# Optimization experiments

Measured on AMD Instinct MI355X. Metric: run time of the kernel, lower is better.

Reference implementation:

```python
import jax, jax.numpy as jnp
import numpy as np

B = 16
COUNTS = np.array([6, 14, 10, 8, 16, 12, 9, 11, 7, 13, 10, 10, 8, 12, 6, 8], dtype=np.int64)  # sum=160, max=16
INPUT_DIM = 1024
D_IN = 834   # num_features_mixed4f + 2
G = 256      # num_features_gcn
NG = 4       # num_graphs
T, H, W = 8, 14, 14


def setup_inputs() -> dict:
    key = jax.random.key(0)
    ks = jax.random.split(key, 7)
    total = int(COUNTS.sum())
    return {
        "actor_features": jax.random.normal(ks[0], (total, INPUT_DIM), dtype=jnp.float32),
        "feature_map": jax.random.normal(ks[1], (B, D_IN, T, H, W), dtype=jnp.float32),
        "W_a": jax.random.normal(ks[2], (NG, G, INPUT_DIM), dtype=jnp.float32) * 0.02,
        "b_a": jnp.zeros((NG, G), dtype=jnp.float32),
        "W_c": jax.random.normal(ks[3], (NG, G, D_IN), dtype=jnp.float32) * 0.02,
        "b_c": jnp.zeros((NG, G), dtype=jnp.float32),
        "W_h": jax.random.normal(ks[4], (NG, G, G), dtype=jnp.float32) * 0.02,
        "num_actors_list": COUNTS,
        "return_features": 0,
    }


def _ragged_indices(counts):
    # static (concrete) ragged bookkeeping
    counts = np.asarray(counts)
    Bn = counts.shape[0]
    Nmax = int(counts.max())
    offsets = np.concatenate([np.zeros(1, np.int64), np.cumsum(counts)[:-1]])
    n = np.arange(Nmax)
    pad_idx = offsets[:, None] + np.minimum(n[None, :], counts[:, None] - 1)  # [B, Nmax]
    valid = (n[None, :] < counts[:, None])                                     # [B, Nmax]
    unpad_b = np.repeat(np.arange(Bn), counts)
    unpad_n = np.concatenate([np.arange(c) for c in counts])
    return pad_idx, valid, unpad_b, unpad_n


def reference(actor_features, feature_map, W_a, b_a, W_c, b_c, W_h,
              num_actors_list, return_features):
    pad_idx, valid, unpad_b, unpad_n = _ragged_indices(num_actors_list)
    valid_f = jnp.asarray(valid, actor_features.dtype)
    Bn = feature_map.shape[0]

    # actor embedding for all graphs: [total, ng, G]
    emb = jnp.einsum('td,gfd->tgf', actor_features, W_a) + b_a[None]
    # pad to [B, Nmax, ng, G]; zero padded slots (matches pad_sequence)
    padded = emb[pad_idx] * valid_f[:, :, None, None]

    # 1x1x1 conv == channel matmul over flattened spatio-temporal grid S=T*H*W
    fm = feature_map.reshape(Bn, feature_map.shape[1], -1)            # [B, C, S]
    ctx = jnp.einsum('bcs,gfc->bgfs', fm, W_c) + b_c[None, :, :, None]  # [B, ng, G, S]

    # adjacency: actor x context similarities, softmax over context locations
    adj = jnp.einsum('bngf,bgfs->bgns', padded, ctx)                  # [B, ng, Nmax, S]
    adj = jax.nn.softmax(adj, axis=-1)
    adj = adj * valid_f[:, None, :, None]                             # masked_fill pad rows -> 0

    # aggregate context + residual
    upd = jnp.einsum('bgns,bgfs->bngf', adj, ctx) + padded            # [B, Nmax, ng, G]

    # unpad back to ragged flat [total, ng, G] (dropout is identity in eval)
    flat = upd[unpad_b, unpad_n]
    out = jax.nn.relu(jnp.einsum('tgf,ghf->tgh', flat, W_h))          # head_linear + relu

    # func == 'concat': cat over graphs along feature dim -> [total, ng*G]
    return out.reshape(out.shape[0], -1)
```

## Files before the change

### kernel.cpp

```cpp
#include <hip/hip_runtime.h>

#define TOTAL   160
#define NMAX    16
#define INDIM   1024
#define DIN     834
#define KPAD    864
#define GF      256
#define SS      1568
#define SPAD    1664
#define CROW    264

__constant__ int c_counts[16] = {6,14,10,8,16,12,9,11,7,13,10,10,8,12,6,8};
__constant__ int c_offs[16]   = {0,6,20,30,38,54,66,75,86,93,106,116,126,134,146,152};
__constant__ int c_t0[4] = {0, 12, 24, 36};
__constant__ int c_t1[4] = {12, 24, 36, 49};

using bf16x8 = __attribute__((ext_vector_type(8))) short;
using f32x4  = __attribute__((ext_vector_type(4))) float;
using us4    = __attribute__((ext_vector_type(4))) unsigned short;

__device__ inline unsigned short f2bf(float f) {
  union { float f; unsigned u; } v; v.f = f;
  const unsigned u = v.u;
  return (unsigned short)((u + 0x7FFFu + ((u >> 16) & 1u)) >> 16);
}
__device__ inline float bf2f(unsigned short h) {
  union { unsigned u; float f; } v; v.u = ((unsigned)h) << 16; return v.f;
}

__global__ __launch_bounds__(256) void prep(const float* __restrict__ Wc,
                                            unsigned short* __restrict__ Ah,
                                            const float* __restrict__ Wh,
                                            unsigned short* __restrict__ Wh_h) {
  const int bid = blockIdx.x, tid = threadIdx.x;
  if (bid < 3456) {
    const int idx = bid * 256 + tid;
    const int k = idx % KPAD, gm = idx / KPAD;
    Ah[idx] = (k < DIN) ? f2bf(Wc[gm * DIN + k]) : (unsigned short)0;
  } else {
    const int i = (bid - 3456) * 256 + tid;
    const float4 v = reinterpret_cast<const float4*>(Wh)[i];
    us4 o; o[0] = f2bf(v.x); o[1] = f2bf(v.y); o[2] = f2bf(v.z); o[3] = f2bf(v.w);
    reinterpret_cast<us4*>(Wh_h)[i] = o;
  }
}

__global__ __launch_bounds__(256) void fm_to_bf16T(const float* __restrict__ fm,
                                                   unsigned short* __restrict__ BhT) {
  __shared__ float tile[32][33];
  const int b  = blockIdx.z;
  const int k0 = blockIdx.y * 32;
  const int s0 = blockIdx.x * 32;
  const int tx = threadIdx.x & 31, ty = threadIdx.x >> 5;
  const float* src = fm + (size_t)b * DIN * SS;
  #pragma unroll
  for (int r = 0; r < 4; ++r) {
    const int k = k0 + ty + r * 8;
    tile[ty + r * 8][tx] = (k < DIN) ? src[(size_t)k * SS + s0 + tx] : 0.f;
  }
  __syncthreads();
  unsigned short* dst = BhT + (size_t)b * SS * KPAD;
  #pragma unroll
  for (int r = 0; r < 4; ++r) {
    const int s = s0 + ty + r * 8;
    dst[(size_t)s * KPAD + k0 + tx] = f2bf(tile[tx][ty + r * 8]);
  }
}

__global__ __launch_bounds__(256, 3) void ctx_mfma(const unsigned short* __restrict__ Ah,
                                                   const unsigned short* __restrict__ BhT,
                                                   const float* __restrict__ b_c,
                                                   unsigned short* __restrict__ ctxT) {
  __shared__ unsigned short As[128 * 40];
  __shared__ unsigned short Bs[128 * 40];
  const int z = blockIdx.z, g = z >> 4, b = z & 15;
  const int n0 = blockIdx.x * 128;
  const int m0 = blockIdx.y * 128;
  const int tid = threadIdx.x;
  const int wave = tid >> 6, lane = tid & 63;
  const int wm = (wave >> 1) * 64, wn = (wave & 1) * 64;
  const int quad = lane >> 4, lr = lane & 15;

  const unsigned short* Ag = BhT + (size_t)b * SS * KPAD;
  const unsigned short* Bg = Ah + (size_t)g * 256 * KPAD + (size_t)n0 * KPAD;

  const int c0 = tid, c1 = tid + 256;
  const int r0 = c0 >> 2, ko0 = (c0 & 3) * 8;
  const int r1 = c1 >> 2, ko1 = (c1 & 3) * 8;

  f32x4 acc[4][4];
  #pragma unroll
  for (int i = 0; i < 4; ++i)
    #pragma unroll
    for (int j = 0; j < 4; ++j) acc[i][j] = (f32x4){0.f, 0.f, 0.f, 0.f};

  uint4 ra0, ra1, rb0, rb1;
  {
    ra0 = *reinterpret_cast<const uint4*>(Ag + (size_t)(m0 + r0) * KPAD + ko0);
    ra1 = *reinterpret_cast<const uint4*>(Ag + (size_t)(m0 + r1) * KPAD + ko1);
    rb0 = *reinterpret_cast<const uint4*>(Bg + (size_t)r0 * KPAD + ko0);
    rb1 = *reinterpret_cast<const uint4*>(Bg + (size_t)r1 * KPAD + ko1);
  }

  for (int kt = 0; kt < 27; ++kt) {
    __syncthreads();
    *reinterpret_cast<uint4*>(&As[r0 * 40 + ko0]) = ra0;
    *reinterpret_cast<uint4*>(&As[r1 * 40 + ko1]) = ra1;
    *reinterpret_cast<uint4*>(&Bs[r0 * 40 + ko0]) = rb0;
    *reinterpret_cast<uint4*>(&Bs[r1 * 40 + ko1]) = rb1;
    __syncthreads();
    if (kt < 26) {
      const int k0 = (kt + 1) * 32;
      ra0 = *reinterpret_cast<const uint4*>(Ag + (size_t)(m0 + r0) * KPAD + k0 + ko0);
      ra1 = *reinterpret_cast<const uint4*>(Ag + (size_t)(m0 + r1) * KPAD + k0 + ko1);
      rb0 = *reinterpret_cast<const uint4*>(Bg + (size_t)r0 * KPAD + k0 + ko0);
      rb1 = *reinterpret_cast<const uint4*>(Bg + (size_t)r1 * KPAD + k0 + ko1);
    }
    bf16x8 af[4], bfr[4];
    #pragma unroll
    for (int i = 0; i < 4; ++i)
      af[i] = *reinterpret_cast<const bf16x8*>(&As[(wm + i * 16 + lr) * 40 + quad * 8]);
    #pragma unroll
    for (int j = 0; j < 4; ++j)
      bfr[j] = *reinterpret_cast<const bf16x8*>(&Bs[(wn + j * 16 + lr) * 40 + quad * 8]);
    #pragma unroll
    for (int i = 0; i < 4; ++i)
      #pragma unroll
      for (int j = 0; j < 4; ++j)
        acc[i][j] = __builtin_amdgcn_mfma_f32_16x16x32_bf16(af[i], bfr[j], acc[i][j], 0, 0, 0);
  }

  unsigned short* Cz = ctxT + (size_t)z * SPAD * GF;
  const float* bias = b_c + g * GF;
  #pragma unroll
  for (int j = 0; j < 4; ++j) {
    const int n = n0 + wn + j * 16 + lr;
    const float bv = bias[n];
    #pragma unroll
    for (int i = 0; i < 4; ++i) {
      #pragma unroll
      for (int reg = 0; reg < 4; ++reg) {
        const int m = m0 + wm + i * 16 + quad * 4 + reg;
        Cz[(size_t)m * GF + n] = f2bf(acc[i][j][reg] + bv);
      }
    }
  }
}

__global__ __launch_bounds__(256) void emb_mfma(const float* __restrict__ actor,
                                                const float* __restrict__ Wa,
                                                const float* __restrict__ b_a,
                                                float* __restrict__ emb,
                                                unsigned short* __restrict__ emb_h) {
  __shared__ unsigned short As[64 * 40];
  __shared__ unsigned short Bs[64 * 40];
  const int n0 = blockIdx.x * 64, m0 = blockIdx.y * 64;
  const int tid = threadIdx.x;
  const int wave = tid >> 6, lane = tid & 63;
  const int wm = (wave >> 1) * 32, wn = (wave & 1) * 32;
  const int quad = lane >> 4, lr = lane & 15;
  const int r = tid >> 2, ko = (tid & 3) * 8;
  const bool mval = (m0 + r < TOTAL);

  f32x4 acc[2][2];
  #pragma unroll
  for (int i = 0; i < 2; ++i)
    #pragma unroll
    for (int j = 0; j < 2; ++j) acc[i][j] = (f32x4){0.f, 0.f, 0.f, 0.f};

  const float4 zf4 = {0.f, 0.f, 0.f, 0.f};
  float4 ra0, ra1, rb0, rb1;
  ra0 = mval ? *reinterpret_cast<const float4*>(actor + (size_t)(m0 + r) * INDIM + ko) : zf4;
  ra1 = mval ? *reinterpret_cast<const float4*>(actor + (size_t)(m0 + r) * INDIM + ko + 4) : zf4;
  rb0 = *reinterpret_cast<const float4*>(Wa + (size_t)(n0 + r) * INDIM + ko);
  rb1 = *reinterpret_cast<const float4*>(Wa + (size_t)(n0 + r) * INDIM + ko + 4);

  for (int kt = 0; kt < 32; ++kt) {
    __syncthreads();
    {
      us4 a0, a1, b0, b1;
      a0[0]=f2bf(ra0.x); a0[1]=f2bf(ra0.y); a0[2]=f2bf(ra0.z); a0[3]=f2bf(ra0.w);
      a1[0]=f2bf(ra1.x); a1[1]=f2bf(ra1.y); a1[2]=f2bf(ra1.z); a1[3]=f2bf(ra1.w);
      b0[0]=f2bf(rb0.x); b0[1]=f2bf(rb0.y); b0[2]=f2bf(rb0.z); b0[3]=f2bf(rb0.w);
      b1[0]=f2bf(rb1.x); b1[1]=f2bf(rb1.y); b1[2]=f2bf(rb1.z); b1[3]=f2bf(rb1.w);
      *reinterpret_cast<us4*>(&As[r * 40 + ko])     = a0;
      *reinterpret_cast<us4*>(&As[r * 40 + ko + 4]) = a1;
      *reinterpret_cast<us4*>(&Bs[r * 40 + ko])     = b0;
      *reinterpret_cast<us4*>(&Bs[r * 40 + ko + 4]) = b1;
    }
    __syncthreads();
    if (kt < 31) {
      const int k0 = (kt + 1) * 32;
      ra0 = mval ? *reinterpret_cast<const float4*>(actor + (size_t)(m0 + r) * INDIM + k0 + ko) : zf4;
      ra1 = mval ? *reinterpret_cast<const float4*>(actor + (size_t)(m0 + r) * INDIM + k0 + ko + 4) : zf4;
      rb0 = *reinterpret_cast<const float4*>(Wa + (size_t)(n0 + r) * INDIM + k0 + ko);
      rb1 = *reinterpret_cast<const float4*>(Wa + (size_t)(n0 + r) * INDIM + k0 + ko + 4);
    }
    bf16x8 af[2], bfr[2];
    #pragma unroll
    for (int i = 0; i < 2; ++i)
      af[i] = *reinterpret_cast<const bf16x8*>(&As[(wm + i * 16 + lr) * 40 + quad * 8]);
    #pragma unroll
    for (int j = 0; j < 2; ++j)
      bfr[j] = *reinterpret_cast<const bf16x8*>(&Bs[(wn + j * 16 + lr) * 40 + quad * 8]);
    #pragma unroll
    for (int i = 0; i < 2; ++i)
      #pragma unroll
      for (int j = 0; j < 2; ++j)
        acc[i][j] = __builtin_amdgcn_mfma_f32_16x16x32_bf16(af[i], bfr[j], acc[i][j], 0, 0, 0);
  }

  #pragma unroll
  for (int i = 0; i < 2; ++i) {
    #pragma unroll
    for (int reg = 0; reg < 4; ++reg) {
      const int m = m0 + wm + i * 16 + quad * 4 + reg;
      if (m >= TOTAL) continue;
      #pragma unroll
      for (int j = 0; j < 2; ++j) {
        const int n = n0 + wn + j * 16 + lr;
        const float v = acc[i][j][reg] + b_a[n];
        emb[(size_t)m * INDIM + n] = v;
        emb_h[(size_t)m * INDIM + n] = f2bf(v);
      }
    }
  }
}

__global__ __launch_bounds__(256) void att_part(
    const unsigned short* __restrict__ ctxT,
    const unsigned short* __restrict__ emb_h,
    float* __restrict__ Opart,
    float* __restrict__ Spart)
{
  __shared__ unsigned short Cs[4][32 * CROW];
  __shared__ float Ps[4][32][20];
  __shared__ float walpha[4][16];
  __shared__ float wms[4][16], wls[4][16];
  const int sc = blockIdx.x, z = blockIdx.y;
  const int g = z >> 4, b = z & 15;
  const int count = c_counts[b], off = c_offs[b];
  const int t0 = c_t0[sc], t1 = c_t1[sc];
  const int tid = threadIdx.x, wave = tid >> 6, lane = tid & 63;
  const int quad = lane >> 4, lr = lane & 15;
  const unsigned short* Az = ctxT + (size_t)z * SPAD * GF;
  const bool bvalid = (lr < count);
  const unsigned short* Brow = emb_h + (size_t)(off + (bvalid ? lr : 0)) * INDIM + (g << 8);
  unsigned short* myC = &Cs[wave][0];
  const int fbase = quad * 64 + lr * 4;
  const bf16x8 zero8 = (bf16x8)(short)0;

  float O[16][4];
  #pragma unroll
  for (int n = 0; n < 16; ++n)
    #pragma unroll
    for (int j = 0; j < 4; ++j) O[n][j] = 0.f;
  float m_run = -3.0e38f, l_run = 0.f;

  for (int t = t0 + wave; t < t1; t += 4) {
    const int s0 = t * 32;
    #pragma unroll
    for (int q = 0; q < 16; ++q) {
      const int row = 2 * q + (lane >> 5);
      const int col = (lane & 31) * 8;
      const uint4 v = *reinterpret_cast<const uint4*>(Az + (size_t)(s0 + row) * GF + col);
      *reinterpret_cast<uint4*>(&myC[row * CROW + col]) = v;
    }
    f32x4 acc[2] = {(f32x4){0.f,0.f,0.f,0.f}, (f32x4){0.f,0.f,0.f,0.f}};
    #pragma unroll
    for (int kk = 0; kk < 8; ++kk) {
      const int f = kk * 32 + quad * 8;
      bf16x8 bv8 = *reinterpret_cast<const bf16x8*>(Brow + f);
      if (!bvalid) bv8 = zero8;
      #pragma unroll
      for (int i = 0; i < 2; ++i) {
        const bf16x8 av8 = *reinterpret_cast<const bf16x8*>(&myC[(i * 16 + lr) * CROW + f]);
        acc[i] = __builtin_amdgcn_mfma_f32_16x16x32_bf16(av8, bv8, acc[i], 0, 0, 0);
      }
    }
    float mx = acc[0][0];
    #pragma unroll
    for (int i = 0; i < 2; ++i)
      #pragma unroll
      for (int r = 0; r < 4; ++r) mx = fmaxf(mx, acc[i][r]);
    float lsum = 0.f;
    #pragma unroll
    for (int i = 0; i < 2; ++i)
      #pragma unroll
      for (int r = 0; r < 4; ++r) lsum += __expf(acc[i][r] - mx);
    #pragma unroll
    for (int d = 16; d < 64; d <<= 1) {
      const float om = __shfl_xor(mx, d, 64);
      const float ol = __shfl_xor(lsum, d, 64);
      const float M = fmaxf(mx, om);
      lsum = lsum * __expf(mx - M) + ol * __expf(om - M);
      mx = M;
    }
    const float m_new = fmaxf(m_run, mx);
    const float alpha = __expf(m_run - m_new);
    const float beta  = __expf(mx - m_new);
    l_run = alpha * l_run + beta * lsum;
    m_run = m_new;
    if (lane < 16) walpha[wave][lane] = alpha;
    #pragma unroll
    for (int i = 0; i < 2; ++i)
      #pragma unroll
      for (int r = 0; r < 4; ++r) {
        const int sl = i * 16 + quad * 4 + r;
        Ps[wave][sl][lr] = beta * __expf(acc[i][r] - mx);
      }
    float av[16];
    {
      const float4 a0 = *reinterpret_cast<const float4*>(&walpha[wave][0]);
      const float4 a1 = *reinterpret_cast<const float4*>(&walpha[wave][4]);
      const float4 a2 = *reinterpret_cast<const float4*>(&walpha[wave][8]);
      const float4 a3 = *reinterpret_cast<const float4*>(&walpha[wave][12]);
      av[0]=a0.x; av[1]=a0.y; av[2]=a0.z; av[3]=a0.w;
      av[4]=a1.x; av[5]=a1.y; av[6]=a1.z; av[7]=a1.w;
      av[8]=a2.x; av[9]=a2.y; av[10]=a2.z; av[11]=a2.w;
      av[12]=a3.x; av[13]=a3.y; av[14]=a3.z; av[15]=a3.w;
    }
    #pragma unroll
    for (int n = 0; n < 16; ++n)
      #pragma unroll
      for (int j = 0; j < 4; ++j) O[n][j] *= av[n];
    for (int s = 0; s < 32; ++s) {
      const float4 p0 = *reinterpret_cast<const float4*>(&Ps[wave][s][0]);
      const float4 p1 = *reinterpret_cast<const float4*>(&Ps[wave][s][4]);
      const float4 p2 = *reinterpret_cast<const float4*>(&Ps[wave][s][8]);
      const float4 p3 = *reinterpret_cast<const float4*>(&Ps[wave][s][12]);
      const us4 cv = *reinterpret_cast<const us4*>(&myC[s * CROW + fbase]);
      const float c0 = bf2f(cv[0]), c1 = bf2f(cv[1]), c2 = bf2f(cv[2]), c3 = bf2f(cv[3]);
      const float pn[16] = {p0.x,p0.y,p0.z,p0.w, p1.x,p1.y,p1.z,p1.w,
                            p2.x,p2.y,p2.z,p2.w, p3.x,p3.y,p3.z,p3.w};
      #pragma unroll
      for (int n = 0; n < 16; ++n) {
        O[n][0] = fmaf(pn[n], c0, O[n][0]);
        O[n][1] = fmaf(pn[n], c1, O[n][1]);
        O[n][2] = fmaf(pn[n], c2, O[n][2]);
        O[n][3] = fmaf(pn[n], c3, O[n][3]);
      }
    }
  }

  if (lane < 16) { wms[wave][lane] = m_run; wls[wave][lane] = l_run; }
  __syncthreads();
  float* Ob = reinterpret_cast<float*>(&Cs[wave][0]);
  #pragma unroll
  for (int n = 0; n < 16; ++n) {
    const float Mb = fmaxf(fmaxf(wms[0][n], wms[1][n]), fmaxf(wms[2][n], wms[3][n]));
    const float e = __expf(wms[wave][n] - Mb);
    #pragma unroll
    for (int j = 0; j < 4; ++j) Ob[n * 256 + fbase + j] = O[n][j] * e;
  }
  __syncthreads();
  float* Op = Opart + ((size_t)z * 4 + sc) * 4096;
  #pragma unroll
  for (int nn = 0; nn < 4; ++nn) {
    const int n = wave * 4 + nn;
    float4 v = {0.f, 0.f, 0.f, 0.f};
    #pragma unroll
    for (int w = 0; w < 4; ++w) {
      const float4 x = *reinterpret_cast<const float4*>(
          reinterpret_cast<const float*>(&Cs[w][0]) + n * 256 + fbase);
      v.x += x.x; v.y += x.y; v.z += x.z; v.w += x.w;
    }
    *reinterpret_cast<float4*>(Op + n * 256 + fbase) = v;
  }
  if (wave == 0 && lane < 16) {
    const int n = lane;
    const float Mb = fmaxf(fmaxf(wms[0][n], wms[1][n]), fmaxf(wms[2][n], wms[3][n]));
    float Lb = 0.f;
    #pragma unroll
    for (int w = 0; w < 4; ++w) Lb += wls[w][n] * __expf(wms[w][n] - Mb);
    Spart[((size_t)z * 4 + sc) * 32 + n]      = Mb;
    Spart[((size_t)z * 4 + sc) * 32 + 16 + n] = Lb;
  }
}

__global__ __launch_bounds__(256) void att_combine(
    const float* __restrict__ Opart, const float* __restrict__ Spart,
    const float* __restrict__ emb, unsigned short* __restrict__ flat_h) {
  const int z = blockIdx.x, n = blockIdx.y;
  const int g = z >> 4, b = z & 15;
  const int count = c_counts[b], off = c_offs[b];
  if (n >= count) return;
  const int f = threadIdx.x;
  float M = -3.0e38f;
  #pragma unroll
  for (int sc = 0; sc < 4; ++sc)
    M = fmaxf(M, Spart[((size_t)z * 4 + sc) * 32 + n]);
  float L = 0.f, acc = 0.f;
  #pragma unroll
  for (int sc = 0; sc < 4; ++sc) {
    const float e = __expf(Spart[((size_t)z * 4 + sc) * 32 + n] - M);
    L += e * Spart[((size_t)z * 4 + sc) * 32 + 16 + n];
    acc += e * Opart[((size_t)z * 4 + sc) * 4096 + n * 256 + f];
  }
  const int t = off + n;
  const int col = (g << 8) + f;
  flat_h[t * INDIM + col] = f2bf(acc / L + emb[t * INDIM + col]);
}

__global__ __launch_bounds__(256) void head_mfma(const unsigned short* __restrict__ flat_h,
                                                 const unsigned short* __restrict__ Wh_h,
                                                 float* __restrict__ out) {
  __shared__ unsigned short As[64 * 40];
  __shared__ unsigned short Bs[64 * 40];
  const int g = blockIdx.z;
  const int n0 = blockIdx.x * 64, m0 = blockIdx.y * 64;
  const int tid = threadIdx.x;
  const int wave = tid >> 6, lane = tid & 63;
  const int wm = (wave >> 1) * 32, wn = (wave & 1) * 32;
  const int quad = lane >> 4, lr = lane & 15;
  const int r = tid >> 2, ko = (tid & 3) * 8;

  const unsigned short* Ag = flat_h + (size_t)m0 * INDIM + g * GF;
  const unsigned short* Bg = Wh_h + (size_t)g * GF * GF + (size_t)n0 * GF;

  f32x4 acc[2][2];
  #pragma unroll
  for (int i = 0; i < 2; ++i)
    #pragma unroll
    for (int j = 0; j < 2; ++j) acc[i][j] = (f32x4){0.f, 0.f, 0.f, 0.f};

  const uint4 zero4 = {0u, 0u, 0u, 0u};
  uint4 ra, rb;
  ra = (m0 + r < TOTAL) ? *reinterpret_cast<const uint4*>(Ag + (size_t)r * INDIM + ko) : zero4;
  rb = *reinterpret_cast<const uint4*>(Bg + (size_t)r * GF + ko);

  for (int kt = 0; kt < 8; ++kt) {
    __syncthreads();
    *reinterpret_cast<uint4*>(&As[r * 40 + ko]) = ra;
    *reinterpret_cast<uint4*>(&Bs[r * 40 + ko]) = rb;
    __syncthreads();
    if (kt < 7) {
      const int k0 = (kt + 1) * 32;
      ra = (m0 + r < TOTAL) ? *reinterpret_cast<const uint4*>(Ag + (size_t)r * INDIM + k0 + ko) : zero4;
      rb = *reinterpret_cast<const uint4*>(Bg + (size_t)r * GF + k0 + ko);
    }
    bf16x8 af[2], bfr[2];
    #pragma unroll
    for (int i = 0; i < 2; ++i)
      af[i] = *reinterpret_cast<const bf16x8*>(&As[(wm + i * 16 + lr) * 40 + quad * 8]);
    #pragma unroll
    for (int j = 0; j < 2; ++j)
      bfr[j] = *reinterpret_cast<const bf16x8*>(&Bs[(wn + j * 16 + lr) * 40 + quad * 8]);
    #pragma unroll
    for (int i = 0; i < 2; ++i)
      #pragma unroll
      for (int j = 0; j < 2; ++j)
        acc[i][j] = __builtin_amdgcn_mfma_f32_16x16x32_bf16(af[i], bfr[j], acc[i][j], 0, 0, 0);
  }

  #pragma unroll
  for (int i = 0; i < 2; ++i) {
    #pragma unroll
    for (int reg = 0; reg < 4; ++reg) {
      const int m = m0 + wm + i * 16 + quad * 4 + reg;
      if (m >= TOTAL) continue;
      #pragma unroll
      for (int j = 0; j < 2; ++j) {
        const int n = n0 + wn + j * 16 + lr;
        out[(size_t)m * INDIM + g * GF + n] = fmaxf(acc[i][j][reg], 0.f);
      }
    }
  }
}

extern "C" void kernel_launch(void* const* d_in, const int* in_sizes, int n_in,
                              void* d_out, int out_size, void* d_ws, size_t ws_size,
                              hipStream_t stream) {
  (void)in_sizes; (void)n_in; (void)out_size; (void)ws_size;
  const float* actor = (const float*)d_in[0];
  const float* fmap  = (const float*)d_in[1];
  const float* W_a   = (const float*)d_in[2];
  const float* b_a   = (const float*)d_in[3];
  const float* W_c   = (const float*)d_in[4];
  const float* b_c   = (const float*)d_in[5];
  const float* W_h   = (const float*)d_in[6];
  float* out = (float*)d_out;
  char* ws = (char*)d_ws;

  float* emb             = (float*)(ws);
  unsigned short* flat_h = (unsigned short*)(ws + 655360);
  unsigned short* emb_h  = (unsigned short*)(ws + 983040);
  float* Spart           = (float*)(ws + 1310720);
  float* Opart           = (float*)(ws + 1343488);
  unsigned short* ctxT   = (unsigned short*)(ws + 18120704);
  unsigned short* Ah     = (unsigned short*)(ws + 72646656);
  unsigned short* BhT    = (unsigned short*)(ws + 74416128);
  unsigned short* Wh_h   = (unsigned short*)(ws + 117768192);

  hipLaunchKernelGGL(prep, dim3(3712), dim3(256), 0, stream, W_c, Ah, W_h, Wh_h);
  hipLaunchKernelGGL(fm_to_bf16T, dim3(49, 27, 16), dim3(256), 0, stream, fmap, BhT);

  hipLaunchKernelGGL(emb_mfma, dim3(16, 3), dim3(256), 0, stream,
                     actor, W_a, b_a, emb, emb_h);

  hipLaunchKernelGGL(ctx_mfma, dim3(2, 13, 64), dim3(256), 0, stream, Ah, BhT, b_c, ctxT);

  hipLaunchKernelGGL(att_part, dim3(4, 64), dim3(256), 0, stream,
                     ctxT, emb_h, Opart, Spart);

  hipLaunchKernelGGL(att_combine, dim3(64, 16), dim3(256), 0, stream,
                     Opart, Spart, emb, flat_h);

  hipLaunchKernelGGL(head_mfma, dim3(4, 3, 4), dim3(256), 0, stream,
                     flat_h, Wh_h, out);
}
```

Measured before the change: 317.8 us.

## Split attention into 8 spatial chunks and double-buffer ctx GEMM prefetch

The attention partial kernel now splits the spatial axis into 8 chunks instead of 4, doubling the grid to 512 blocks so more of the GPU is busy, and the combine kernel merges 8 partial softmax states. The ctx GEMM unrolls its K loop by two with two register prefetch sets, loading tiles two steps ahead to hide global latency. Workspace is repacked so Opart aliases the BhT buffer, which is dead by the time att_part runs. The extra register buffers may reduce occupancy in ctx_mfma, and the combine step reads more partials.

New measurement: 316.3 us. About the same (-0.5%).

```diff
diff --git a/kernel.cpp b/kernel.cpp
--- a/kernel.cpp
+++ b/kernel.cpp
@@ -12,8 +12,8 @@
 
 __constant__ int c_counts[16] = {6,14,10,8,16,12,9,11,7,13,10,10,8,12,6,8};
 __constant__ int c_offs[16]   = {0,6,20,30,38,54,66,75,86,93,106,116,126,134,146,152};
-__constant__ int c_t0[4] = {0, 12, 24, 36};
-__constant__ int c_t1[4] = {12, 24, 36, 49};
+__constant__ int c_t0[8] = {0, 6, 12, 18, 25, 31, 37, 43};
+__constant__ int c_t1[8] = {6, 12, 18, 25, 31, 37, 43, 49};
 
 using bf16x8 = __attribute__((ext_vector_type(8))) short;
 using f32x4  = __attribute__((ext_vector_type(4))) float;
@@ -67,6 +67,35 @@
   }
 }
 
+#define CTX_STEP(RA0, RA1, RB0, RB1, KT)                                               \
+  {                                                                                    \
+    __syncthreads();                                                                   \
+    *reinterpret_cast<uint4*>(&As[r0 * 40 + ko0]) = RA0;                               \
+    *reinterpret_cast<uint4*>(&As[r1 * 40 + ko1]) = RA1;                               \
+    *reinterpret_cast<uint4*>(&Bs[r0 * 40 + ko0]) = RB0;                               \
+    *reinterpret_cast<uint4*>(&Bs[r1 * 40 + ko1]) = RB1;                               \
+    __syncthreads();                                                                   \
+    if ((KT) + 2 < 27) {                                                               \
+      const int k0n = ((KT) + 2) * 32;                                                 \
+      RA0 = *reinterpret_cast<const uint4*>(Ag + (size_t)(m0 + r0) * KPAD + k0n + ko0);\
+      RA1 = *reinterpret_cast<const uint4*>(Ag + (size_t)(m0 + r1) * KPAD + k0n + ko1);\
+      RB0 = *reinterpret_cast<const uint4*>(Bg + (size_t)r0 * KPAD + k0n + ko0);       \
+      RB1 = *reinterpret_cast<const uint4*>(Bg + (size_t)r1 * KPAD + k0n + ko1);       \
+    }                                                                                  \
+    bf16x8 af[4], bfr[4];                                                              \
+    _Pragma("unroll")                                                                  \
+    for (int i = 0; i < 4; ++i)                                                        \
+      af[i] = *reinterpret_cast<const bf16x8*>(&As[(wm + i * 16 + lr) * 40 + quad * 8]); \
+    _Pragma("unroll")                                                                  \
+    for (int j = 0; j < 4; ++j)                                                        \
+      bfr[j] = *reinterpret_cast<const bf16x8*>(&Bs[(wn + j * 16 + lr) * 40 + quad * 8]); \
+    _Pragma("unroll")                                                                  \
+    for (int i = 0; i < 4; ++i)                                                        \
+      _Pragma("unroll")                                                                \
+      for (int j = 0; j < 4; ++j)                                                      \
+        acc[i][j] = __builtin_amdgcn_mfma_f32_16x16x32_bf16(af[i], bfr[j], acc[i][j], 0, 0, 0); \
+  }
+
 __global__ __launch_bounds__(256, 3) void ctx_mfma(const unsigned short* __restrict__ Ah,
                                                    const unsigned short* __restrict__ BhT,
                                                    const float* __restrict__ b_c,
@@ -94,40 +123,19 @@
     #pragma unroll
     for (int j = 0; j < 4; ++j) acc[i][j] = (f32x4){0.f, 0.f, 0.f, 0.f};
 
-  uint4 ra0, ra1, rb0, rb1;
-  {
-    ra0 = *reinterpret_cast<const uint4*>(Ag + (size_t)(m0 + r0) * KPAD + ko0);
-    ra1 = *reinterpret_cast<const uint4*>(Ag + (size_t)(m0 + r1) * KPAD + ko1);
-    rb0 = *reinterpret_cast<const uint4*>(Bg + (size_t)r0 * KPAD + ko0);
-    rb1 = *reinterpret_cast<const uint4*>(Bg + (size_t)r1 * KPAD + ko1);
-  }
-
-  for (int kt = 0; kt < 27; ++kt) {
-    __syncthreads();
-    *reinterpret_cast<uint4*>(&As[r0 * 40 + ko0]) = ra0;
-    *reinterpret_cast<uint4*>(&As[r1 * 40 + ko1]) = ra1;
-    *reinterpret_cast<uint4*>(&Bs[r0 * 40 + ko0]) = rb0;
-    *reinterpret_cast<uint4*>(&Bs[r1 * 40 + ko1]) = rb1;
-    __syncthreads();
-    if (kt < 26) {
-      const int k0 = (kt + 1) * 32;
-      ra0 = *reinterpret_cast<const uint4*>(Ag + (size_t)(m0 + r0) * KPAD + k0 + ko0);
-      ra1 = *reinterpret_cast<const uint4*>(Ag + (size_t)(m0 + r1) * KPAD + k0 + ko1);
-      rb0 = *reinterpret_cast<const uint4*>(Bg + (size_t)r0 * KPAD + k0 + ko0);
-      rb1 = *reinterpret_cast<const uint4*>(Bg + (size_t)r1 * KPAD + k0 + ko1);
-    }
-    bf16x8 af[4], bfr[4];
-    #pragma unroll
-    for (int i = 0; i < 4; ++i)
-      af[i] = *reinterpret_cast<const bf16x8*>(&As[(wm + i * 16 + lr) * 40 + quad * 8]);
-    #pragma unroll
-    for (int j = 0; j < 4; ++j)
-      bfr[j] = *reinterpret_cast<const bf16x8*>(&Bs[(wn + j * 16 + lr) * 40 + quad * 8]);
-    #pragma unroll
-    for (int i = 0; i < 4; ++i)
-      #pragma unroll
-      for (int j = 0; j < 4; ++j)
-        acc[i][j] = __builtin_amdgcn_mfma_f32_16x16x32_bf16(af[i], bfr[j], acc[i][j], 0, 0, 0);
+  uint4 ra0a, ra1a, rb0a, rb1a, ra0b, ra1b, rb0b, rb1b;
+  ra0a = *reinterpret_cast<const uint4*>(Ag + (size_t)(m0 + r0) * KPAD + ko0);
+  ra1a = *reinterpret_cast<const uint4*>(Ag + (size_t)(m0 + r1) * KPAD + ko1);
+  rb0a = *reinterpret_cast<const uint4*>(Bg + (size_t)r0 * KPAD + ko0);
+  rb1a = *reinterpret_cast<const uint4*>(Bg + (size_t)r1 * KPAD + ko1);
+  ra0b = *reinterpret_cast<const uint4*>(Ag + (size_t)(m0 + r0) * KPAD + 32 + ko0);
+  ra1b = *reinterpret_cast<const uint4*>(Ag + (size_t)(m0 + r1) * KPAD + 32 + ko1);
+  rb0b = *reinterpret_cast<const uint4*>(Bg + (size_t)r0 * KPAD + 32 + ko0);
+  rb1b = *reinterpret_cast<const uint4*>(Bg + (size_t)r1 * KPAD + 32 + ko1);
+
+  for (int kt = 0; kt < 27; kt += 2) {
+    CTX_STEP(ra0a, ra1a, rb0a, rb1a, kt);
+    if (kt + 1 < 27) CTX_STEP(ra0b, ra1b, rb0b, rb1b, kt + 1);
   }
 
   unsigned short* Cz = ctxT + (size_t)z * SPAD * GF;
@@ -354,7 +362,7 @@
     for (int j = 0; j < 4; ++j) Ob[n * 256 + fbase + j] = O[n][j] * e;
   }
   __syncthreads();
-  float* Op = Opart + ((size_t)z * 4 + sc) * 4096;
+  float* Op = Opart + ((size_t)z * 8 + sc) * 4096;
   #pragma unroll
   for (int nn = 0; nn < 4; ++nn) {
     const int n = wave * 4 + nn;
@@ -373,8 +381,8 @@
     float Lb = 0.f;
     #pragma unroll
     for (int w = 0; w < 4; ++w) Lb += wls[w][n] * __expf(wms[w][n] - Mb);
-    Spart[((size_t)z * 4 + sc) * 32 + n]      = Mb;
-    Spart[((size_t)z * 4 + sc) * 32 + 16 + n] = Lb;
+    Spart[((size_t)z * 8 + sc) * 32 + n]      = Mb;
+    Spart[((size_t)z * 8 + sc) * 32 + 16 + n] = Lb;
   }
 }
 
@@ -388,14 +396,14 @@
   const int f = threadIdx.x;
   float M = -3.0e38f;
   #pragma unroll
-  for (int sc = 0; sc < 4; ++sc)
-    M = fmaxf(M, Spart[((size_t)z * 4 + sc) * 32 + n]);
+  for (int sc = 0; sc < 8; ++sc)
+    M = fmaxf(M, Spart[((size_t)z * 8 + sc) * 32 + n]);
   float L = 0.f, acc = 0.f;
   #pragma unroll
-  for (int sc = 0; sc < 4; ++sc) {
-    const float e = __expf(Spart[((size_t)z * 4 + sc) * 32 + n] - M);
-    L += e * Spart[((size_t)z * 4 + sc) * 32 + 16 + n];
-    acc += e * Opart[((size_t)z * 4 + sc) * 4096 + n * 256 + f];
+  for (int sc = 0; sc < 8; ++sc) {
+    const float e = __expf(Spart[((size_t)z * 8 + sc) * 32 + n] - M);
+    L += e * Spart[((size_t)z * 8 + sc) * 32 + 16 + n];
+    acc += e * Opart[((size_t)z * 8 + sc) * 4096 + n * 256 + f];
   }
   const int t = off + n;
   const int col = (g << 8) + f;
@@ -486,11 +494,11 @@
   unsigned short* flat_h = (unsigned short*)(ws + 655360);
   unsigned short* emb_h  = (unsigned short*)(ws + 983040);
   float* Spart           = (float*)(ws + 1310720);
-  float* Opart           = (float*)(ws + 1343488);
-  unsigned short* ctxT   = (unsigned short*)(ws + 18120704);
-  unsigned short* Ah     = (unsigned short*)(ws + 72646656);
-  unsigned short* BhT    = (unsigned short*)(ws + 74416128);
-  unsigned short* Wh_h   = (unsigned short*)(ws + 117768192);
+  unsigned short* ctxT   = (unsigned short*)(ws + 1376256);
+  unsigned short* Ah     = (unsigned short*)(ws + 55902208);
+  unsigned short* BhT    = (unsigned short*)(ws + 57671680);
+  float* Opart           = (float*)(ws + 57671680);
+  unsigned short* Wh_h   = (unsigned short*)(ws + 101023744);
 
   hipLaunchKernelGGL(prep, dim3(3712), dim3(256), 0, stream, W_c, Ah, W_h, Wh_h);
   hipLaunchKernelGGL(fm_to_bf16T, dim3(49, 27, 16), dim3(256), 0, stream, fmap, BhT);
@@ -500,7 +508,7 @@
 
   hipLaunchKernelGGL(ctx_mfma, dim3(2, 13, 64), dim3(256), 0, stream, Ah, BhT, b_c, ctxT);
 
-  hipLaunchKernelGGL(att_part, dim3(4, 64), dim3(256), 0, stream,
+  hipLaunchKernelGGL(att_part, dim3(8, 64), dim3(256), 0, stream,
                      ctxT, emb_h, Opart, Spart);
 
   hipLaunchKernelGGL(att_combine, dim3(64, 16), dim3(256), 0, stream,
```
